# Performance work log

Measured on AMD Instinct MI355X. Metric: run time of the kernel, lower is better.

The kernel has to match this reference:

```python
import jax, jax.numpy as jnp
import numpy as np

B, E, CIN, COUT, K, H, W = 32, 5, 256, 256, 3, 56, 56
R = 4
SCALING = 16.0 / R  # lora_alpha / r


def setup_inputs() -> dict:
    key = jax.random.key(0)
    k1, k2, k3, k4, k5 = jax.random.split(key, 5)
    x = jax.random.normal(k1, (B, CIN, H, W), dtype=jnp.float32)
    scores = jax.random.normal(k2, (B, E), dtype=jnp.float32)
    weight = jax.random.normal(k3, (COUT, CIN, K, K), dtype=jnp.float32) * 0.02
    lora_A = jax.random.normal(k4, (E, R * K, CIN * K), dtype=jnp.float32) * 0.02
    lora_B = jax.random.normal(k5, (E, COUT * K, R * K), dtype=jnp.float32) * 0.02
    return {"x": x, "scores": scores, "weight": weight, "lora_A": lora_A, "lora_B": lora_B}


def reference(x, scores, weight, lora_A, lora_B):
    b = x.shape[0]
    # hard top-1 expert one-hot with straight-through estimator (GetMask backward: d scores = d one_hot)
    hard = jax.nn.one_hot(jnp.argmax(scores, axis=1), scores.shape[1], dtype=scores.dtype)  # [B,E]
    one_hot = scores + jax.lax.stop_gradient(hard - scores)
    # per-expert LoRA delta weights: [E, O*K, I*K] -> [E, O, I, K, K]
    delta = jnp.einsum('eor,eri->eoi', lora_B, lora_A)
    delta = delta.reshape(delta.shape[0], *weight.shape) * SCALING
    # per-sample aggregated weights: [B, O, I, K, K]
    agg = weight[None] + jnp.einsum('be,eoikl->boikl', one_hot, delta)
    # grouped conv2d with groups = batch
    out = jax.lax.conv_general_dilated(
        x.reshape(1, -1, x.shape[2], x.shape[3]),          # [1, B*Cin, H, W]
        agg.reshape(-1, *agg.shape[-3:]),                   # [B*O, Cin, K, K]
        window_strides=(1, 1),
        padding=((1, 1), (1, 1)),
        feature_group_count=b,
        dimension_numbers=('NCHW', 'OIHW', 'NCHW'),
    )
    return out.reshape(b, -1, out.shape[2], out.shape[3])
```

## Files before the change

### kernel.cpp

```cpp
#include <hip/hip_runtime.h>
#include <hip/hip_bf16.h>

#define BB    32
#define EE    5
#define HH    56
#define WW    56
#define KKC   2304
#define SCAL  4.0f

typedef __attribute__((ext_vector_type(8))) short short8;
typedef __attribute__((ext_vector_type(4))) float f32x4;

#define WF2_PER_E  (9 * 8 * 256 * 32)
#define XP2_PER_BC (58 * 58 * 32)

__device__ __forceinline__ void gload_lds16(const void* g, void* l) {
    __builtin_amdgcn_global_load_lds(
        (const __attribute__((address_space(1))) unsigned int*)g,
        (__attribute__((address_space(3))) unsigned int*)l, 16, 0, 0);
}

__device__ __forceinline__ unsigned short f2bf(float f) {
    unsigned int u = __float_as_uint(f);
    return (unsigned short)((u + 0x7FFFu + ((u >> 16) & 1u)) >> 16);
}

__global__ __launch_bounds__(256) void lora_prep_kernel(
    const float* __restrict__ weight,
    const float* __restrict__ lora_A,
    const float* __restrict__ lora_B,
    unsigned short* __restrict__ Wf2)
{
    const int co = blockIdx.x;
    const int e  = blockIdx.y;
    const int ci = threadIdx.x;

    __shared__ float As[12 * 768];
    __shared__ float Bs[3][12];
    for (int i = threadIdx.x; i < 12 * 768; i += 256)
        As[i] = lora_A[e * 12 * 768 + i];
    if (threadIdx.x < 36)
        Bs[threadIdx.x / 12][threadIdx.x % 12] =
            lora_B[((size_t)e * 768 + co * 3 + threadIdx.x / 12) * 12 + threadIdx.x % 12];
    __syncthreads();

    const float* wrow = weight + (size_t)co * KKC + ci * 9;
    const int cic = ci >> 5, ci32 = ci & 31;
    #pragma unroll
    for (int tap = 0; tap < 9; ++tap) {
        int idx  = ci * 9 + tap;
        int q    = idx / 768;
        int i768 = idx - q * 768;
        float acc = 0.f;
        #pragma unroll
        for (int r = 0; r < 12; ++r)
            acc += Bs[q][r] * As[r * 768 + i768];
        float v = wrow[tap] + SCAL * acc;
        Wf2[((size_t)((e * 9 + tap) * 8 + cic)) * 8192 + co * 32 + ci32] = f2bf(v);
    }
}

__global__ __launch_bounds__(256) void lora_xpose_kernel(
    const float* __restrict__ x,
    unsigned short* __restrict__ xpad2)
{
    const int rp  = blockIdx.x;
    const int b   = blockIdx.y;
    const int tid = threadIdx.x;
    unsigned short* xp = xpad2 + (size_t)b * 8 * XP2_PER_BC;
    const uint4 z4 = {0u, 0u, 0u, 0u};

    if (rp == 0 || rp == 57) {
        for (int t = tid; t < 1856; t += 256) {
            int cic = t / 232, q = t % 232;
            ((uint4*)(xp + ((size_t)cic * 3364 + rp * 58) * 32))[q] = z4;
        }
        return;
    }
    if (tid < 64) {
        int cic = tid >> 3, which = (tid >> 2) & 1, q = tid & 3;
        ((uint4*)(xp + ((size_t)cic * 3364 + rp * 58 + (which ? 57 : 0)) * 32))[q] = z4;
    }

    const int row = rp - 1;
    const float* xb = x + (size_t)b * 256 * 3136 + row * 56;
    __shared__ float xt[32][60];

    for (int cic = 0; cic < 8; ++cic) {
        __syncthreads();
        #pragma unroll
        for (int it = 0; it < 7; ++it) {
            int t = it * 256 + tid;
            int i = t / 56, c = t % 56;
            xt[i][c] = xb[(size_t)(cic * 32 + i) * 3136 + c];
        }
        __syncthreads();
        if (tid < 224) {
            int c  = tid >> 2, gq = tid & 3;
            int cp = c + 1;
            int gphys = gq ^ ((cp >> 1) & 3);
            unsigned int w[4];
            #pragma unroll
            for (int j = 0; j < 4; ++j) {
                unsigned short lo = f2bf(xt[gq * 8 + 2 * j + 0][c]);
                unsigned short hi = f2bf(xt[gq * 8 + 2 * j + 1][c]);
                w[j] = (unsigned int)lo | ((unsigned int)hi << 16);
            }
            uint4 pk; pk.x = w[0]; pk.y = w[1]; pk.z = w[2]; pk.w = w[3];
            *(uint4*)(xp + ((size_t)cic * 3364 + rp * 58 + cp) * 32 + gphys * 8) = pk;
        }
    }
}

__global__ __launch_bounds__(256, 2) void lora_conv_mfma_kernel(
    const unsigned short* __restrict__ xpad2,
    const unsigned short* __restrict__ Wf2,
    const float* __restrict__ scores,
    float* __restrict__ out)
{
    const int y0   = blockIdx.x * 4;
    const int co0  = blockIdx.y * 128;
    const int b    = blockIdx.z;
    const int tid  = threadIdx.x;
    const int wave = tid >> 6;
    const int lane = tid & 63;
    const int ln15 = lane & 15;
    const int quad = lane >> 4;
    const int wm2  = (wave & 1) * 64;
    const int wn2  = (wave >> 1) * 112;

    __shared__ short8 Xlds[2][1392];
    __shared__ int sExp;

    if (tid == 0) {
        const float* s = scores + b * EE;
        int best = 0; float bv = s[0];
        #pragma unroll
        for (int j = 1; j < EE; ++j) { float v = s[j]; if (v > bv) { bv = v; best = j; } }
        sExp = best;
    }

    const unsigned short* xsrc0 = xpad2 + (size_t)b * 8 * XP2_PER_BC + y0 * 58 * 32;

    auto stage = [&](int cic, int buf) {
        const unsigned short* src = xsrc0 + (size_t)cic * XP2_PER_BC;
        char* dst = (char*)&Xlds[buf][0];
        #pragma unroll
        for (int i = 0; i < 5; ++i) {
            int G = i * 256 + tid;
            gload_lds16(src + (size_t)G * 8, dst + (size_t)G * 16);
        }
        if (tid < 112) {
            int G = 1280 + tid;
            gload_lds16(src + (size_t)G * 8, dst + (size_t)G * 16);
        }
    };

    stage(0, 0);
    __syncthreads();
    const int e = sExp;

    const unsigned short* Wb =
        Wf2 + (size_t)e * WF2_PER_E + (co0 + wm2 + ln15) * 32 + quad * 8;

    int pgk[7][3];
    #pragma unroll
    for (int tn = 0; tn < 7; ++tn) {
        int pos = wn2 + tn * 16 + ln15;
        int r = pos / 56, c = pos % 56;
        #pragma unroll
        for (int k2 = 0; k2 < 3; ++k2) {
            int cc = c + k2;
            int g  = quad ^ ((cc >> 1) & 3);
            pgk[tn][k2] = (r * 232 + cc * 4 + g) * 16;
        }
    }

    f32x4 acc[4][7];
    #pragma unroll
    for (int tm = 0; tm < 4; ++tm)
        #pragma unroll
        for (int tn = 0; tn < 7; ++tn)
            acc[tm][tn] = (f32x4){0.f, 0.f, 0.f, 0.f};

    short8 Acur[4], Anext[4];

    for (int cic = 0; cic < 8; ++cic) {
        const unsigned short* Wc = Wb + cic * 8192;
        #pragma unroll
        for (int tm = 0; tm < 4; ++tm)
            Acur[tm] = *(const short8*)(Wc + tm * 512);

        const char* Xb = (const char*)&Xlds[cic & 1][0];
        #pragma unroll
        for (int tap = 0; tap < 9; ++tap) {
            if (tap == 1 && cic < 7) stage(cic + 1, (cic & 1) ^ 1);
            if (tap < 8) {
                #pragma unroll
                for (int tm = 0; tm < 4; ++tm)
                    Anext[tm] = *(const short8*)(Wc + (tap + 1) * 65536 + tm * 512);
            }
            const int k1 = tap / 3, k2 = tap % 3;
            #pragma unroll
            for (int tn = 0; tn < 7; ++tn) {
                short8 bfr = *(const short8*)(Xb + pgk[tn][k2] + k1 * 3712);
                #pragma unroll
                for (int tm = 0; tm < 4; ++tm)
                    acc[tm][tn] = __builtin_amdgcn_mfma_f32_16x16x32_bf16(
                        Acur[tm], bfr, acc[tm][tn], 0, 0, 0);
            }
            #pragma unroll
            for (int tm = 0; tm < 4; ++tm) Acur[tm] = Anext[tm];
        }
        if (cic < 7) __syncthreads();
    }

    #pragma unroll
    for (int tm = 0; tm < 4; ++tm) {
        #pragma unroll
        for (int tn = 0; tn < 7; ++tn) {
            int n = wn2 + tn * 16 + ln15;
            int r = n / 56, c = n % 56;
            #pragma unroll
            for (int reg = 0; reg < 4; ++reg) {
                int m = co0 + wm2 + tm * 16 + quad * 4 + reg;
                out[(((size_t)b * 256 + m) * HH + y0 + r) * WW + c] = acc[tm][tn][reg];
            }
        }
    }
}

extern "C" void kernel_launch(void* const* d_in, const int* in_sizes, int n_in,
                              void* d_out, int out_size, void* d_ws, size_t ws_size,
                              hipStream_t stream) {
    const float* x      = (const float*)d_in[0];
    const float* scores = (const float*)d_in[1];
    const float* weight = (const float*)d_in[2];
    const float* lora_A = (const float*)d_in[3];
    const float* lora_B = (const float*)d_in[4];
    float* out = (float*)d_out;

    char* ws = (char*)d_ws;
    unsigned short* Wf2   = (unsigned short*)(ws + 256);
    unsigned short* xpad2 = (unsigned short*)(ws + 256 + (size_t)EE * WF2_PER_E * 2);

    lora_prep_kernel<<<dim3(256, EE), 256, 0, stream>>>(weight, lora_A, lora_B, Wf2);
    lora_xpose_kernel<<<dim3(58, BB), 256, 0, stream>>>(x, xpad2);
    lora_conv_mfma_kernel<<<dim3(14, 2, BB), 256, 0, stream>>>(xpad2, Wf2, scores, out);
}
```

Measured before the change: 321.3 us.

## Merge prep kernels, deepen weight prefetch, raise MFMA priority, transpose LDS tile

The LoRA weight-prep kernel and the input transpose/pad kernel become a single launch with a blockIdx split and a shared-memory union, saving one launch and letting the two jobs run concurrently. In the conv kernel, weight fragments are now prefetched two taps ahead across cic boundaries, next-channel staging starts at tap 0, and the MFMA section runs under s_setprio(1). The per-tile LDS offsets are packed into fewer registers. The transpose tile is stored column-major with padding to change the LDS bank pattern. The extra prefetch buffer adds register pressure under the 2-waves launch bound and could cause spills.

Measured after the change: 298.1 us. 7.2% less time.

```diff
diff --git a/kernel.cpp b/kernel.cpp
--- a/kernel.cpp
+++ b/kernel.cpp
@@ -14,6 +14,9 @@
 #define WF2_PER_E  (9 * 8 * 256 * 32)
 #define XP2_PER_BC (58 * 58 * 32)
 
+#define NXPB (58 * BB)
+#define NPRB (256 * EE)
+
 __device__ __forceinline__ void gload_lds16(const void* g, void* l) {
     __builtin_amdgcn_global_load_lds(
         (const __attribute__((address_space(1))) unsigned int*)g,
@@ -25,48 +28,53 @@
     return (unsigned short)((u + 0x7FFFu + ((u >> 16) & 1u)) >> 16);
 }
 
-__global__ __launch_bounds__(256) void lora_prep_kernel(
+__global__ __launch_bounds__(256) void lora_prep_xpose_kernel(
+    const float* __restrict__ x,
     const float* __restrict__ weight,
     const float* __restrict__ lora_A,
     const float* __restrict__ lora_B,
-    unsigned short* __restrict__ Wf2)
-{
-    const int co = blockIdx.x;
-    const int e  = blockIdx.y;
-    const int ci = threadIdx.x;
-
-    __shared__ float As[12 * 768];
-    __shared__ float Bs[3][12];
-    for (int i = threadIdx.x; i < 12 * 768; i += 256)
-        As[i] = lora_A[e * 12 * 768 + i];
-    if (threadIdx.x < 36)
-        Bs[threadIdx.x / 12][threadIdx.x % 12] =
-            lora_B[((size_t)e * 768 + co * 3 + threadIdx.x / 12) * 12 + threadIdx.x % 12];
-    __syncthreads();
-
-    const float* wrow = weight + (size_t)co * KKC + ci * 9;
-    const int cic = ci >> 5, ci32 = ci & 31;
-    #pragma unroll
-    for (int tap = 0; tap < 9; ++tap) {
-        int idx  = ci * 9 + tap;
-        int q    = idx / 768;
-        int i768 = idx - q * 768;
-        float acc = 0.f;
-        #pragma unroll
-        for (int r = 0; r < 12; ++r)
-            acc += Bs[q][r] * As[r * 768 + i768];
-        float v = wrow[tap] + SCAL * acc;
-        Wf2[((size_t)((e * 9 + tap) * 8 + cic)) * 8192 + co * 32 + ci32] = f2bf(v);
-    }
-}
-
-__global__ __launch_bounds__(256) void lora_xpose_kernel(
-    const float* __restrict__ x,
+    unsigned short* __restrict__ Wf2,
     unsigned short* __restrict__ xpad2)
 {
-    const int rp  = blockIdx.x;
-    const int b   = blockIdx.y;
+    __shared__ union ShU {
+        struct { float As[12 * 768]; float Bs[3][12]; } p;
+        float xt[56][33];
+    } sh;
     const int tid = threadIdx.x;
+
+    if (blockIdx.x >= NXPB) {
+        const int pid = blockIdx.x - NXPB;
+        const int co  = pid & 255;
+        const int e   = pid >> 8;
+        const int ci  = tid;
+
+        for (int i = tid; i < 12 * 768; i += 256)
+            sh.p.As[i] = lora_A[e * 12 * 768 + i];
+        if (tid < 36)
+            sh.p.Bs[tid / 12][tid % 12] =
+                lora_B[((size_t)e * 768 + co * 3 + tid / 12) * 12 + tid % 12];
+        __syncthreads();
+
+        const float* wrow = weight + (size_t)co * KKC + ci * 9;
+        const int cic = ci >> 5, ci32 = ci & 31;
+        #pragma unroll
+        for (int tap = 0; tap < 9; ++tap) {
+            int idx  = ci * 9 + tap;
+            int q    = idx / 768;
+            int i768 = idx - q * 768;
+            float acc = 0.f;
+            #pragma unroll
+            for (int r = 0; r < 12; ++r)
+                acc += sh.p.Bs[q][r] * sh.p.As[r * 768 + i768];
+            float v = wrow[tap] + SCAL * acc;
+            Wf2[((size_t)((e * 9 + tap) * 8 + cic)) * 8192 + co * 32 + ci32] = f2bf(v);
+        }
+        return;
+    }
+
+    const int bid = blockIdx.x;
+    const int b   = bid / 58;
+    const int rp  = bid - b * 58;
     unsigned short* xp = xpad2 + (size_t)b * 8 * XP2_PER_BC;
     const uint4 z4 = {0u, 0u, 0u, 0u};
 
@@ -84,15 +92,14 @@
 
     const int row = rp - 1;
     const float* xb = x + (size_t)b * 256 * 3136 + row * 56;
-    __shared__ float xt[32][60];
 
     for (int cic = 0; cic < 8; ++cic) {
         __syncthreads();
         #pragma unroll
         for (int it = 0; it < 7; ++it) {
             int t = it * 256 + tid;
-            int i = t / 56, c = t % 56;
-            xt[i][c] = xb[(size_t)(cic * 32 + i) * 3136 + c];
+            int i = t / 56, c = t - i * 56;
+            sh.xt[c][i] = xb[(size_t)(cic * 32 + i) * 3136 + c];
         }
         __syncthreads();
         if (tid < 224) {
@@ -102,8 +109,8 @@
             unsigned int w[4];
             #pragma unroll
             for (int j = 0; j < 4; ++j) {
-                unsigned short lo = f2bf(xt[gq * 8 + 2 * j + 0][c]);
-                unsigned short hi = f2bf(xt[gq * 8 + 2 * j + 1][c]);
+                unsigned short lo = f2bf(sh.xt[c][gq * 8 + 2 * j + 0]);
+                unsigned short hi = f2bf(sh.xt[c][gq * 8 + 2 * j + 1]);
                 w[j] = (unsigned int)lo | ((unsigned int)hi << 16);
             }
             uint4 pk; pk.x = w[0]; pk.y = w[1]; pk.z = w[2]; pk.w = w[3];
@@ -163,17 +170,20 @@
     const unsigned short* Wb =
         Wf2 + (size_t)e * WF2_PER_E + (co0 + wm2 + ln15) * 32 + quad * 8;
 
-    int pgk[7][3];
+    int pg01[7], pg2[7];
     #pragma unroll
     for (int tn = 0; tn < 7; ++tn) {
         int pos = wn2 + tn * 16 + ln15;
-        int r = pos / 56, c = pos % 56;
+        int r = pos / 56, c = pos - r * 56;
+        int o[3];
         #pragma unroll
         for (int k2 = 0; k2 < 3; ++k2) {
             int cc = c + k2;
             int g  = quad ^ ((cc >> 1) & 3);
-            pgk[tn][k2] = (r * 232 + cc * 4 + g) * 16;
-        }
+            o[k2] = (r * 232 + cc * 4 + g) * 16;
+        }
+        pg01[tn] = o[0] | (o[1] << 16);
+        pg2[tn]  = o[2];
     }
 
     f32x4 acc[4][7];
@@ -183,34 +193,44 @@
         for (int tn = 0; tn < 7; ++tn)
             acc[tm][tn] = (f32x4){0.f, 0.f, 0.f, 0.f};
 
-    short8 Acur[4], Anext[4];
+    short8 A0[4], A1[4], A2[4];
+    #pragma unroll
+    for (int tm = 0; tm < 4; ++tm) {
+        A0[tm] = *(const short8*)(Wb + 0 * 65536 + tm * 512);
+        A1[tm] = *(const short8*)(Wb + 1 * 65536 + tm * 512);
+    }
 
     for (int cic = 0; cic < 8; ++cic) {
         const unsigned short* Wc = Wb + cic * 8192;
-        #pragma unroll
-        for (int tm = 0; tm < 4; ++tm)
-            Acur[tm] = *(const short8*)(Wc + tm * 512);
-
         const char* Xb = (const char*)&Xlds[cic & 1][0];
         #pragma unroll
         for (int tap = 0; tap < 9; ++tap) {
-            if (tap == 1 && cic < 7) stage(cic + 1, (cic & 1) ^ 1);
-            if (tap < 8) {
+            if (tap == 0 && cic < 7) stage(cic + 1, (cic & 1) ^ 1);
+            if (tap < 7) {
                 #pragma unroll
                 for (int tm = 0; tm < 4; ++tm)
-                    Anext[tm] = *(const short8*)(Wc + (tap + 1) * 65536 + tm * 512);
+                    A2[tm] = *(const short8*)(Wc + (tap + 2) * 65536 + tm * 512);
+            } else if (cic < 7) {
+                #pragma unroll
+                for (int tm = 0; tm < 4; ++tm)
+                    A2[tm] = *(const short8*)(Wc + 8192 + (tap - 7) * 65536 + tm * 512);
             }
             const int k1 = tap / 3, k2 = tap % 3;
+            __builtin_amdgcn_s_setprio(1);
             #pragma unroll
             for (int tn = 0; tn < 7; ++tn) {
-                short8 bfr = *(const short8*)(Xb + pgk[tn][k2] + k1 * 3712);
+                int off = (k2 == 0) ? (pg01[tn] & 0xffff)
+                        : (k2 == 1) ? (pg01[tn] >> 16)
+                                    : pg2[tn];
+                short8 bfr = *(const short8*)(Xb + off + k1 * 3712);
                 #pragma unroll
                 for (int tm = 0; tm < 4; ++tm)
                     acc[tm][tn] = __builtin_amdgcn_mfma_f32_16x16x32_bf16(
-                        Acur[tm], bfr, acc[tm][tn], 0, 0, 0);
-            }
-            #pragma unroll
-            for (int tm = 0; tm < 4; ++tm) Acur[tm] = Anext[tm];
+                        A0[tm], bfr, acc[tm][tn], 0, 0, 0);
+            }
+            __builtin_amdgcn_s_setprio(0);
+            #pragma unroll
+            for (int tm = 0; tm < 4; ++tm) { A0[tm] = A1[tm]; A1[tm] = A2[tm]; }
         }
         if (cic < 7) __syncthreads();
     }
@@ -220,7 +240,7 @@
         #pragma unroll
         for (int tn = 0; tn < 7; ++tn) {
             int n = wn2 + tn * 16 + ln15;
-            int r = n / 56, c = n % 56;
+            int r = n / 56, c = n - r * 56;
             #pragma unroll
             for (int reg = 0; reg < 4; ++reg) {
                 int m = co0 + wm2 + tm * 16 + quad * 4 + reg;
@@ -244,7 +264,7 @@
     unsigned short* Wf2   = (unsigned short*)(ws + 256);
     unsigned short* xpad2 = (unsigned short*)(ws + 256 + (size_t)EE * WF2_PER_E * 2);
 
-    lora_prep_kernel<<<dim3(256, EE), 256, 0, stream>>>(weight, lora_A, lora_B, Wf2);
-    lora_xpose_kernel<<<dim3(58, BB), 256, 0, stream>>>(x, xpad2);
+    lora_prep_xpose_kernel<<<dim3(NXPB + NPRB), 256, 0, stream>>>(
+        x, weight, lora_A, lora_B, Wf2, xpad2);
     lora_conv_mfma_kernel<<<dim3(14, 2, BB), 256, 0, stream>>>(xpad2, Wf2, scores, out);
 }
```
